# Optimization experiments

Hardware: AMD Instinct MI355X
Metric: run time of the kernel (lower is better)

## Reference

```python
import jax, jax.numpy as jnp
import numpy as np

N_NODES = 20000
N_EDGES = 160000
N_GRAPHS = 64
X_DIM = 9
E_DIM = 1
U_RAW = 4096
U_DIM = 256
E_HID = 1024
E_OUT = 512
N_HID = 512
N_OUT = 1


def _lin_params(k, fan_in, fan_out):
    kw, kb = jax.random.split(k)
    bound = 1.0 / np.sqrt(fan_in)
    W = jax.random.uniform(kw, (fan_in, fan_out), jnp.float32, -bound, bound)
    b = jax.random.uniform(kb, (fan_out,), jnp.float32, -bound, bound)
    return W, b


def setup_inputs() -> dict:
    key = jax.random.key(0)
    ks = jax.random.split(key, 16)
    x = jax.random.normal(ks[0], (N_NODES, X_DIM), jnp.float32)
    edge_attr = jax.random.normal(ks[1], (N_EDGES, E_DIM), jnp.float32)
    u = jax.random.normal(ks[2], (N_GRAPHS, U_RAW), jnp.float32)
    edge_index = jax.random.randint(ks[3], (2, N_EDGES), 0, N_NODES, jnp.int64)
    batch = jax.random.randint(ks[4], (N_NODES,), 0, N_GRAPHS, jnp.int64)

    Wsel, bsel = _lin_params(ks[5], U_RAW, U_DIM)
    e_in = E_DIM + 2 * X_DIM + U_DIM  # 275
    eW1, eb1 = _lin_params(ks[6], e_in, E_HID)
    eW2, eb2 = _lin_params(ks[7], E_HID, E_HID)
    eW3, eb3 = _lin_params(ks[8], E_HID, E_HID)
    eW4, eb4 = _lin_params(ks[9], E_HID, E_HID)
    eW5, eb5 = _lin_params(ks[10], E_HID, E_OUT)
    n1W1, n1b1 = _lin_params(ks[11], E_OUT + X_DIM, N_HID)  # 521
    n1W2, n1b2 = _lin_params(ks[12], N_HID, N_HID)
    n2W1, n2b1 = _lin_params(ks[13], X_DIM + N_HID + U_DIM, N_HID)  # 777
    n2W2, n2b2 = _lin_params(ks[14], N_HID, N_OUT)

    return dict(x=x, edge_attr=edge_attr, u=u, edge_index=edge_index, batch=batch,
                Wsel=Wsel, bsel=bsel,
                eW1=eW1, eb1=eb1, eW2=eW2, eb2=eb2, eW3=eW3, eb3=eb3,
                eW4=eW4, eb4=eb4, eW5=eW5, eb5=eb5,
                n1W1=n1W1, n1b1=n1b1, n1W2=n1W2, n1b2=n1b2,
                n2W1=n2W1, n2b1=n2b1, n2W2=n2W2, n2b2=n2b2)


def _forward(x, edge_attr, u, edge_index, batch,
             Wsel, bsel, eW1, eb1, eW2, eb2, eW3, eb3, eW4, eb4, eW5, eb5,
             n1W1, n1b1, n1W2, n1b2, n2W1, n2b1, n2W2, n2b2):
    relu = jax.nn.relu
    u2 = u @ Wsel + bsel  # [B, 256]
    row, col = edge_index[0], edge_index[1]

    # EdgeModel: cat([src, dest, edge_attr, u[batch[row]]]) -> 5-layer MLP
    e = jnp.concatenate([x[row], x[col], edge_attr, u2[batch[row]]], axis=1)
    e = relu(e @ eW1 + eb1)
    e = relu(e @ eW2 + eb2)
    e = relu(e @ eW3 + eb3)
    e = relu(e @ eW4 + eb4)
    e = e @ eW5 + eb5  # [E, 512]

    # NodeModel: gather x[col], MLP1, scatter_mean over row, MLP2
    h = jnp.concatenate([x[col], e], axis=1)
    h = relu(h @ n1W1 + n1b1)
    h = relu(h @ n1W2 + n1b2)  # [E, 512]
    ssum = jax.ops.segment_sum(h, row, num_segments=x.shape[0])
    cnt = jax.ops.segment_sum(jnp.ones((h.shape[0],), h.dtype), row, num_segments=x.shape[0])
    agg = ssum / jnp.maximum(cnt, 1.0)[:, None]  # scatter_mean

    z = jnp.concatenate([x, agg, u2[batch]], axis=1)
    z = relu(z @ n2W1 + n2b1)
    z = z @ n2W2 + n2b2  # [N, 1]
    return jnp.squeeze(z)


def reference(x, edge_attr, u, edge_index, batch,
              Wsel, bsel, eW1, eb1, eW2, eb2, eW3, eb3, eW4, eb4, eW5, eb5,
              n1W1, n1b1, n1W2, n1b2, n2W1, n2b1, n2W2, n2b2):
    return _forward(x, edge_attr, u, edge_index, batch,
                    Wsel, bsel, eW1, eb1, eW2, eb2, eW3, eb3, eW4, eb4, eW5, eb5,
                    n1W1, n1b1, n1W2, n1b2, n2W1, n2b1, n2W2, n2b2)
```

## Files before the change

kernel.cpp:

```cpp
#include <hip/hip_runtime.h>

typedef _Float16 f16;
typedef __attribute__((ext_vector_type(8))) _Float16 f16x8;
typedef __attribute__((ext_vector_type(4))) float f32x4;

#define E_TOTAL 160000
#define NN 20000
#define NGRAPH 64

__device__ __forceinline__ void gl_lds16(const void* g, void* l) {
    __builtin_amdgcn_global_load_lds((const __attribute__((address_space(1))) void*)g,
                                     (__attribute__((address_space(3))) void*)l, 16, 0, 0);
}

template <int RELU, int AUXU, int AUXX>
__global__ __launch_bounds__(256, 2) void hgemm(
    int M, int N, int K,
    const f16* __restrict__ A, int lda,
    const f16* __restrict__ Bt,
    f16* __restrict__ C, int ldc,
    const float* __restrict__ bias,
    const f16* __restrict__ utab, const int* __restrict__ uidx,
    const float* __restrict__ x9, const int* __restrict__ xidx, const float* __restrict__ W9)
{
    __shared__ __align__(16) char Ash[16384];
    __shared__ __align__(16) char Bsh[16384];
    __shared__ float Ws9[AUXX ? 1152 : 1];
    const int tid  = threadIdx.x;
    const int lane = tid & 63;
    const int w    = tid >> 6;
    const int bm = blockIdx.y * 128;
    const int bn = blockIdx.x * 128;
    const int wm = (w >> 1) * 64;
    const int wn = (w & 1) * 64;
    const int fr = lane & 15;
    const int kq = lane >> 4;

    const char* Ab = (const char*)A;
    const char* Bb = (const char*)Bt;
    const size_t lda2 = (size_t)lda * 2;
    const size_t ldb2 = (size_t)K * 2;

    f32x4 acc[4][4] = {};

    int srow[4], scb[4];
#pragma unroll
    for (int h = 0; h < 4; ++h) {
        int cch = w * 4 + h;
        int L = cch * 1024 + lane * 16;
        int row = L >> 7;
        srow[h] = row;
        scb[h] = (L & 127) ^ ((row & 7) << 4);
    }

    for (int k0 = 0; k0 < K; k0 += 64) {
        __syncthreads();
#pragma unroll
        for (int h = 0; h < 4; ++h) {
            int cch = w * 4 + h;
            gl_lds16(Ab + (size_t)(bm + srow[h]) * lda2 + (size_t)k0 * 2 + scb[h], Ash + cch * 1024);
            gl_lds16(Bb + (size_t)(bn + srow[h]) * ldb2 + (size_t)k0 * 2 + scb[h], Bsh + cch * 1024);
        }
        __syncthreads();
#pragma unroll
        for (int kk = 0; kk < 2; ++kk) {
            const int cb = (kk * 32 + kq * 8) * 2;
            f16x8 av[4], bv[4];
#pragma unroll
            for (int m = 0; m < 4; ++m) {
                int r = wm + m * 16 + fr;
                av[m] = *(const f16x8*)(Ash + r * 128 + (cb ^ ((r & 7) << 4)));
            }
#pragma unroll
            for (int n = 0; n < 4; ++n) {
                int r = wn + n * 16 + fr;
                bv[n] = *(const f16x8*)(Bsh + r * 128 + (cb ^ ((r & 7) << 4)));
            }
#pragma unroll
            for (int m = 0; m < 4; ++m)
#pragma unroll
                for (int n = 0; n < 4; ++n)
                    acc[m][n] = __builtin_amdgcn_mfma_f32_16x16x32_f16(av[m], bv[n], acc[m][n], 0, 0, 0);
        }
    }

    if (AUXX) {
        for (int t = tid; t < 9 * 128; t += 256)
            Ws9[t] = W9[(size_t)(t >> 7) * N + bn + (t & 127)];
        __syncthreads();
    }

#pragma unroll
    for (int m = 0; m < 4; ++m) {
        int r0 = bm + wm + m * 16 + kq * 4;
#pragma unroll
        for (int r = 0; r < 4; ++r) {
            int grow = r0 + r;
            if (grow >= M) continue;
            int ub = 0;
            if (AUXU) ub = uidx[grow];
            float xv[9];
            if (AUXX) {
                int xi = xidx ? xidx[grow] : grow;
#pragma unroll
                for (int q = 0; q < 9; ++q) xv[q] = x9[(size_t)xi * 9 + q];
            }
#pragma unroll
            for (int n = 0; n < 4; ++n) {
                int lcol = wn + n * 16 + fr;
                int col = bn + lcol;
                float v = acc[m][n][r] + bias[col];
                if (AUXU) v += (float)utab[(size_t)ub * N + col];
                if (AUXX) {
                    float s = 0.f;
#pragma unroll
                    for (int q = 0; q < 9; ++q) s = fmaf(xv[q], Ws9[q * 128 + lcol], s);
                    v += s;
                }
                if (RELU) v = fmaxf(v, 0.f);
                C[(size_t)grow * ldc + col] = (f16)v;
            }
        }
    }
}

__global__ void k_wt(const float* __restrict__ W, f16* __restrict__ Wt,
                     int r0, int Ksub, int N, int Kp)
{
    size_t t = (size_t)blockIdx.x * 256 + threadIdx.x;
    if (t >= (size_t)N * Kp) return;
    int n = (int)(t / Kp), k = (int)(t % Kp);
    Wt[t] = (k < Ksub) ? (f16)W[(size_t)(r0 + k) * N + n] : (f16)0.f;
}

__global__ __launch_bounds__(256) void k_u2(const float* __restrict__ u,
                                            const float* __restrict__ Wsel,
                                            const float* __restrict__ bsel,
                                            f16* __restrict__ u2h)
{
    __shared__ float us[4096];
    __shared__ float red[4][64];
    const int g = blockIdx.y;
    const int c0 = blockIdx.x * 64;
    const int col = threadIdx.x & 63;
    const int kp = threadIdx.x >> 6;
    for (int i = threadIdx.x; i < 4096; i += 256) us[i] = u[(size_t)g * 4096 + i];
    __syncthreads();
    float acc = 0.f;
    for (int k = kp * 1024; k < kp * 1024 + 1024; ++k)
        acc = fmaf(us[k], Wsel[(size_t)k * 256 + c0 + col], acc);
    red[kp][col] = acc;
    __syncthreads();
    if (kp == 0) {
        float v = red[0][col] + red[1][col] + red[2][col] + red[3][col] + bsel[c0 + col];
        u2h[(size_t)g * 256 + c0 + col] = (f16)v;
    }
}

__global__ void k_gather19(int e0, int Ce,
                           const float* __restrict__ x, const float* __restrict__ eattr,
                           const int* __restrict__ ei, const int* __restrict__ batch,
                           f16* __restrict__ feat, int* __restrict__ ebat)
{
    size_t t = (size_t)blockIdx.x * 256 + threadIdx.x;
    if (t >= (size_t)Ce * 64) return;
    int i = (int)(t >> 6), j = (int)(t & 63);
    int e = e0 + i;
    float v = 0.f;
    if (j < 9)        v = x[ei[e] * 9 + j];
    else if (j < 18)  v = x[ei[E_TOTAL + e] * 9 + (j - 9)];
    else if (j == 18) v = eattr[e];
    else if (j == 19) ebat[i] = batch[ei[e]];
    feat[t] = (f16)v;
}

__global__ void k_scatter(int e0, int Ce, const f16* __restrict__ h2,
                          const int* __restrict__ ei, float* __restrict__ ssum)
{
    size_t t = (size_t)blockIdx.x * 256 + threadIdx.x;
    if (t >= (size_t)Ce * 512) return;
    int i = (int)(t >> 9), j = (int)(t & 511);
    atomicAdd(ssum + (size_t)ei[e0 + i] * 512 + j, (float)h2[t]);
}

__global__ void k_cnt(const int* __restrict__ ei, float* __restrict__ cnt)
{
    int t = blockIdx.x * 256 + threadIdx.x;
    if (t < E_TOTAL) atomicAdd(cnt + ei[t], 1.0f);
}

__global__ void k_agg(const float* __restrict__ ssum, const float* __restrict__ cnt,
                      f16* __restrict__ agg)
{
    size_t t = (size_t)blockIdx.x * 256 + threadIdx.x;
    if (t >= (size_t)NN * 512) return;
    int n = (int)(t >> 9);
    agg[t] = (f16)(ssum[t] / fmaxf(cnt[n], 1.f));
}

__global__ void k_final(const f16* __restrict__ z1, const float* __restrict__ W,
                        const float* __restrict__ b, float* __restrict__ out)
{
    int gt = blockIdx.x * 256 + threadIdx.x;
    int row = gt >> 6;
    int lane = threadIdx.x & 63;
    if (row >= NN) return;
    float s = 0.f;
#pragma unroll
    for (int c = lane; c < 512; c += 64) s += (float)z1[(size_t)row * 512 + c] * W[c];
#pragma unroll
    for (int off = 32; off; off >>= 1) s += __shfl_down(s, off);
    if (lane == 0) out[row] = s + b[0];
}


extern "C" void kernel_launch(void* const* d_in, const int* in_sizes, int n_in,
                              void* d_out, int out_size, void* d_ws, size_t ws_size,
                              hipStream_t stream)
{
    const float* x     = (const float*)d_in[0];
    const float* eattr = (const float*)d_in[1];
    const float* u     = (const float*)d_in[2];
    const int*   ei    = (const int*)d_in[3];
    const int*   batch = (const int*)d_in[4];
    const float* Wsel  = (const float*)d_in[5];
    const float* bsel  = (const float*)d_in[6];
    const float* eW1 = (const float*)d_in[7],  * eb1 = (const float*)d_in[8];
    const float* eW2 = (const float*)d_in[9],  * eb2 = (const float*)d_in[10];
    const float* eW3 = (const float*)d_in[11], * eb3 = (const float*)d_in[12];
    const float* eW4 = (const float*)d_in[13], * eb4 = (const float*)d_in[14];
    const float* eW5 = (const float*)d_in[15], * eb5 = (const float*)d_in[16];
    const float* n1W1 = (const float*)d_in[17], * n1b1 = (const float*)d_in[18];
    const float* n1W2 = (const float*)d_in[19], * n1b2 = (const float*)d_in[20];
    const float* n2W1 = (const float*)d_in[21], * n2b1 = (const float*)d_in[22];
    const float* n2W2 = (const float*)d_in[23], * n2b2 = (const float*)d_in[24];
    float* out = (float*)d_out;

    char* ws = (char*)d_ws;
    size_t off = 0;
    auto alc = [&](size_t bytes) { char* p = ws + off; off += (bytes + 255) & ~(size_t)255; return p; };

    float* ssum  = (float*)alc((size_t)NN * 512 * 4);
    float* cnt   = (float*)alc((size_t)NN * 4);
    float* zbias = (float*)alc(1024 * 4);
    f16* u2h     = (f16*)alc((size_t)128 * 256 * 2);
    f16* ubias_e = (f16*)alc((size_t)64 * 1024 * 2);
    f16* ubias_n = (f16*)alc((size_t)64 * 512 * 2);
    f16* eW1t19  = (f16*)alc((size_t)1024 * 64 * 2);
    f16* eW1ut   = (f16*)alc((size_t)1024 * 256 * 2);
    f16* eW2t    = (f16*)alc((size_t)1024 * 1024 * 2);
    f16* eW3t    = (f16*)alc((size_t)1024 * 1024 * 2);
    f16* eW4t    = (f16*)alc((size_t)1024 * 1024 * 2);
    f16* eW5t    = (f16*)alc((size_t)512 * 1024 * 2);
    f16* n1W1et  = (f16*)alc((size_t)512 * 512 * 2);
    f16* n1W2t   = (f16*)alc((size_t)512 * 512 * 2);
    f16* n2W1et  = (f16*)alc((size_t)512 * 512 * 2);
    f16* n2W1ut  = (f16*)alc((size_t)512 * 256 * 2);
    f16* agg     = (f16*)alc((size_t)20096 * 512 * 2);
    f16* z1      = (f16*)alc((size_t)20096 * 512 * 2);
    size_t fixed = off;

    size_t per_edge = 64 * 2 + 1024 * 2 + 1024 * 2 + 4;
    size_t avail = ws_size > fixed ? ws_size - fixed : 0;
    long long Cll = (long long)(avail / per_edge);
    int C = (int)((Cll / 128) * 128);
    if (C > E_TOTAL) C = E_TOTAL;
    if (C < 128) C = 128;

    f16* featc = (f16*)(ws + fixed);
    f16* buf1  = featc + (size_t)C * 64;
    f16* buf2  = buf1 + (size_t)C * 1024;
    int* ebat  = (int*)(buf2 + (size_t)C * 1024);

    size_t zlen = (size_t)((char*)zbias - (char*)ssum) + 1024 * 4;
    hipMemsetAsync(ssum, 0, zlen, stream);

    auto wt = [&](const float* W, f16* Wt, int r0, int Ksub, int N, int Kp) {
        size_t tot = (size_t)N * Kp;
        k_wt<<<(unsigned)((tot + 255) / 256), 256, 0, stream>>>(W, Wt, r0, Ksub, N, Kp);
    };
    wt(eW1, eW1t19, 0, 19, 1024, 64);
    wt(eW1, eW1ut, 19, 256, 1024, 256);
    wt(eW2, eW2t, 0, 1024, 1024, 1024);
    wt(eW3, eW3t, 0, 1024, 1024, 1024);
    wt(eW4, eW4t, 0, 1024, 1024, 1024);
    wt(eW5, eW5t, 0, 1024, 512, 1024);
    wt(n1W1, n1W1et, 9, 512, 512, 512);
    wt(n1W2, n1W2t, 0, 512, 512, 512);
    wt(n2W1, n2W1et, 9, 512, 512, 512);
    wt(n2W1, n2W1ut, 521, 256, 512, 256);

    k_u2<<<dim3(4, NGRAPH), 256, 0, stream>>>(u, Wsel, bsel, u2h);
    k_cnt<<<(E_TOTAL + 255) / 256, 256, 0, stream>>>(ei, cnt);

    hgemm<0,0,0><<<dim3(8, 1), 256, 0, stream>>>(64, 1024, 256, u2h, 256, eW1ut,
        ubias_e, 1024, eb1, nullptr, nullptr, nullptr, nullptr, nullptr);
    hgemm<0,0,0><<<dim3(4, 1), 256, 0, stream>>>(64, 512, 256, u2h, 256, n2W1ut,
        ubias_n, 512, n2b1, nullptr, nullptr, nullptr, nullptr, nullptr);

    for (int e0 = 0; e0 < E_TOTAL; e0 += C) {
        int Ce = E_TOTAL - e0 < C ? E_TOTAL - e0 : C;
        int gy = (Ce + 127) / 128;

        k_gather19<<<(unsigned)(((size_t)Ce * 64 + 255) / 256), 256, 0, stream>>>(
            e0, Ce, x, eattr, ei, batch, featc, ebat);

        hgemm<1,1,0><<<dim3(8, gy), 256, 0, stream>>>(Ce, 1024, 64, featc, 64, eW1t19,
            buf1, 1024, zbias, ubias_e, ebat, nullptr, nullptr, nullptr);
        hgemm<1,0,0><<<dim3(8, gy), 256, 0, stream>>>(Ce, 1024, 1024, buf1, 1024, eW2t,
            buf2, 1024, eb2, nullptr, nullptr, nullptr, nullptr, nullptr);
        hgemm<1,0,0><<<dim3(8, gy), 256, 0, stream>>>(Ce, 1024, 1024, buf2, 1024, eW3t,
            buf1, 1024, eb3, nullptr, nullptr, nullptr, nullptr, nullptr);
        hgemm<1,0,0><<<dim3(8, gy), 256, 0, stream>>>(Ce, 1024, 1024, buf1, 1024, eW4t,
            buf2, 1024, eb4, nullptr, nullptr, nullptr, nullptr, nullptr);
        hgemm<0,0,0><<<dim3(4, gy), 256, 0, stream>>>(Ce, 512, 1024, buf2, 1024, eW5t,
            buf1, 512, eb5, nullptr, nullptr, nullptr, nullptr, nullptr);

        hgemm<1,0,1><<<dim3(4, gy), 256, 0, stream>>>(Ce, 512, 512, buf1, 512, n1W1et,
            buf2, 512, n1b1, nullptr, nullptr, x, ei + E_TOTAL + e0, n1W1);
        hgemm<1,0,0><<<dim3(4, gy), 256, 0, stream>>>(Ce, 512, 512, buf2, 512, n1W2t,
            buf1, 512, n1b2, nullptr, nullptr, nullptr, nullptr, nullptr);

        k_scatter<<<(unsigned)(((size_t)Ce * 512 + 255) / 256), 256, 0, stream>>>(
            e0, Ce, buf1, ei, ssum);
    }

    k_agg<<<(unsigned)(((size_t)NN * 512 + 255) / 256), 256, 0, stream>>>(ssum, cnt, agg);
    hgemm<1,1,1><<<dim3(4, 157), 256, 0, stream>>>(NN, 512, 512, agg, 512, n2W1et,
        z1, 512, zbias, ubias_n, batch, x, nullptr, n2W1);
    k_final<<<(NN * 64 + 255) / 256, 256, 0, stream>>>(z1, n2W2, n2b2, out);
}
```

Baseline: 2.588 ms.

## Enlarge GEMM tiles to 256x256 with 512 threads and double-buffered LDS

Replaces the 128x128 / 256-thread hgemm with a 256x256 / 512-thread variant. Each wave now computes a 128x64 sub-tile. LDS is double-buffered: the next K-slice is prefetched with global_load_lds while the current one feeds the MFMAs. Only one barrier per iteration remains, and s_setprio is raised around the MFMA block. The goal is more data reuse per tile and overlap of global loads with compute. In exchange, each block uses about 128KB of LDS, which limits occupancy. With a single barrier, a fast wave may start filling a buffer that slower waves are still reading. Small launches get fewer blocks, and workspace padding is adjusted to 256-row multiples.

```diff
diff --git a/kernel.cpp b/kernel.cpp
--- a/kernel.cpp
+++ b/kernel.cpp
@@ -14,7 +14,7 @@
 }
 
 template <int RELU, int AUXU, int AUXX>
-__global__ __launch_bounds__(256, 2) void hgemm(
+__global__ __launch_bounds__(512, 2) void hgemm2(
     int M, int N, int K,
     const f16* __restrict__ A, int lda,
     const f16* __restrict__ Bt,
@@ -23,16 +23,17 @@
     const f16* __restrict__ utab, const int* __restrict__ uidx,
     const float* __restrict__ x9, const int* __restrict__ xidx, const float* __restrict__ W9)
 {
-    __shared__ __align__(16) char Ash[16384];
-    __shared__ __align__(16) char Bsh[16384];
-    __shared__ float Ws9[AUXX ? 1152 : 1];
+    __shared__ __align__(16) char Ash[2][32768];
+    __shared__ __align__(16) char Bsh[2][32768];
+    __shared__ float Ws9[AUXX ? 2304 : 1];
+
     const int tid  = threadIdx.x;
     const int lane = tid & 63;
     const int w    = tid >> 6;
-    const int bm = blockIdx.y * 128;
-    const int bn = blockIdx.x * 128;
-    const int wm = (w >> 1) * 64;
-    const int wn = (w & 1) * 64;
+    const int bm = blockIdx.y * 256;
+    const int bn = blockIdx.x * 256;
+    const int wm = (w >> 2) * 128;
+    const int wn = (w & 3) * 64;
     const int fr = lane & 15;
     const int kq = lane >> 4;
 
@@ -41,58 +42,83 @@
     const size_t lda2 = (size_t)lda * 2;
     const size_t ldb2 = (size_t)K * 2;
 
-    f32x4 acc[4][4] = {};
-
-    int srow[4], scb[4];
-#pragma unroll
-    for (int h = 0; h < 4; ++h) {
-        int cch = w * 4 + h;
+    f32x4 acc[8][4] = {};
+
+    size_t offA[4], offB[4];
+    int ldsoff[4];
+#pragma unroll
+    for (int i = 0; i < 4; ++i) {
+        int cch = w * 4 + i;
         int L = cch * 1024 + lane * 16;
         int row = L >> 7;
-        srow[h] = row;
-        scb[h] = (L & 127) ^ ((row & 7) << 4);
-    }
-
-    for (int k0 = 0; k0 < K; k0 += 64) {
+        int scb = (L & 127) ^ ((row & 7) << 4);
+        offA[i] = (size_t)(bm + row) * lda2 + scb;
+        offB[i] = (size_t)(bn + row) * ldb2 + scb;
+        ldsoff[i] = cch * 1024;
+    }
+
+    const int NT = K >> 6;
+
+#pragma unroll
+    for (int i = 0; i < 4; ++i) gl_lds16(Ab + offA[i], Ash[0] + ldsoff[i]);
+#pragma unroll
+    for (int i = 0; i < 4; ++i) gl_lds16(Bb + offB[i], Bsh[0] + ldsoff[i]);
+
+    int cur = 0;
+    for (int t = 0; t < NT; ++t) {
+        if (t + 1 < NT) {
+            size_t kb = (size_t)(t + 1) << 7;
+#pragma unroll
+            for (int i = 0; i < 4; ++i) gl_lds16(Ab + offA[i] + kb, Ash[cur ^ 1] + ldsoff[i]);
+#pragma unroll
+            for (int i = 0; i < 4; ++i) gl_lds16(Bb + offB[i] + kb, Bsh[cur ^ 1] + ldsoff[i]);
+            asm volatile("s_waitcnt vmcnt(8)" ::: "memory");
+        } else {
+            asm volatile("s_waitcnt vmcnt(0)" ::: "memory");
+        }
+        __builtin_amdgcn_s_barrier();
+        __builtin_amdgcn_sched_barrier(0);
+
+        const char* As = Ash[cur];
+        const char* Bs = Bsh[cur];
+
+        f16x8 bv[2][4];
+#pragma unroll
+        for (int ks = 0; ks < 2; ++ks) {
+            const int cb = (ks * 32 + kq * 8) * 2;
+#pragma unroll
+            for (int ni = 0; ni < 4; ++ni) {
+                int r = wn + ni * 16 + fr;
+                bv[ks][ni] = *(const f16x8*)(Bs + r * 128 + (cb ^ ((r & 7) << 4)));
+            }
+        }
+        __builtin_amdgcn_s_setprio(1);
+#pragma unroll
+        for (int mi = 0; mi < 8; ++mi) {
+            int r = wm + mi * 16 + fr;
+            int sw = (r & 7) << 4;
+            f16x8 a0 = *(const f16x8*)(As + r * 128 + ((kq * 16) ^ sw));
+            f16x8 a1 = *(const f16x8*)(As + r * 128 + ((64 + kq * 16) ^ sw));
+#pragma unroll
+            for (int ni = 0; ni < 4; ++ni)
+                acc[mi][ni] = __builtin_amdgcn_mfma_f32_16x16x32_f16(a0, bv[0][ni], acc[mi][ni], 0, 0, 0);
+#pragma unroll
+            for (int ni = 0; ni < 4; ++ni)
+                acc[mi][ni] = __builtin_amdgcn_mfma_f32_16x16x32_f16(a1, bv[1][ni], acc[mi][ni], 0, 0, 0);
+        }
+        __builtin_amdgcn_s_setprio(0);
+        cur ^= 1;
+    }
+
+    if (AUXX) {
+        for (int t = tid; t < 9 * 256; t += 512)
+            Ws9[t] = W9[(size_t)(t >> 8) * N + bn + (t & 255)];
         __syncthreads();
-#pragma unroll
-        for (int h = 0; h < 4; ++h) {
-            int cch = w * 4 + h;
-            gl_lds16(Ab + (size_t)(bm + srow[h]) * lda2 + (size_t)k0 * 2 + scb[h], Ash + cch * 1024);
-            gl_lds16(Bb + (size_t)(bn + srow[h]) * ldb2 + (size_t)k0 * 2 + scb[h], Bsh + cch * 1024);
-        }
-        __syncthreads();
-#pragma unroll
-        for (int kk = 0; kk < 2; ++kk) {
-            const int cb = (kk * 32 + kq * 8) * 2;
-            f16x8 av[4], bv[4];
-#pragma unroll
-            for (int m = 0; m < 4; ++m) {
-                int r = wm + m * 16 + fr;
-                av[m] = *(const f16x8*)(Ash + r * 128 + (cb ^ ((r & 7) << 4)));
-            }
-#pragma unroll
-            for (int n = 0; n < 4; ++n) {
-                int r = wn + n * 16 + fr;
-                bv[n] = *(const f16x8*)(Bsh + r * 128 + (cb ^ ((r & 7) << 4)));
-            }
-#pragma unroll
-            for (int m = 0; m < 4; ++m)
-#pragma unroll
-                for (int n = 0; n < 4; ++n)
-                    acc[m][n] = __builtin_amdgcn_mfma_f32_16x16x32_f16(av[m], bv[n], acc[m][n], 0, 0, 0);
-        }
-    }
-
-    if (AUXX) {
-        for (int t = tid; t < 9 * 128; t += 256)
-            Ws9[t] = W9[(size_t)(t >> 7) * N + bn + (t & 127)];
-        __syncthreads();
-    }
-
-#pragma unroll
-    for (int m = 0; m < 4; ++m) {
-        int r0 = bm + wm + m * 16 + kq * 4;
+    }
+
+#pragma unroll
+    for (int mi = 0; mi < 8; ++mi) {
+        int r0 = bm + wm + mi * 16 + kq * 4;
 #pragma unroll
         for (int r = 0; r < 4; ++r) {
             int grow = r0 + r;
@@ -106,15 +132,15 @@
                 for (int q = 0; q < 9; ++q) xv[q] = x9[(size_t)xi * 9 + q];
             }
 #pragma unroll
-            for (int n = 0; n < 4; ++n) {
-                int lcol = wn + n * 16 + fr;
+            for (int ni = 0; ni < 4; ++ni) {
+                int lcol = wn + ni * 16 + fr;
                 int col = bn + lcol;
-                float v = acc[m][n][r] + bias[col];
+                float v = acc[mi][ni][r] + bias[col];
                 if (AUXU) v += (float)utab[(size_t)ub * N + col];
                 if (AUXX) {
                     float s = 0.f;
 #pragma unroll
-                    for (int q = 0; q < 9; ++q) s = fmaf(xv[q], Ws9[q * 128 + lcol], s);
+                    for (int q = 0; q < 9; ++q) s = fmaf(xv[q], Ws9[q * 256 + lcol], s);
                     v += s;
                 }
                 if (RELU) v = fmaxf(v, 0.f);
@@ -243,7 +269,7 @@
     float* ssum  = (float*)alc((size_t)NN * 512 * 4);
     float* cnt   = (float*)alc((size_t)NN * 4);
     float* zbias = (float*)alc(1024 * 4);
-    f16* u2h     = (f16*)alc((size_t)128 * 256 * 2);
+    f16* u2h     = (f16*)alc((size_t)256 * 256 * 2);
     f16* ubias_e = (f16*)alc((size_t)64 * 1024 * 2);
     f16* ubias_n = (f16*)alc((size_t)64 * 512 * 2);
     f16* eW1t19  = (f16*)alc((size_t)1024 * 64 * 2);
@@ -256,16 +282,16 @@
     f16* n1W2t   = (f16*)alc((size_t)512 * 512 * 2);
     f16* n2W1et  = (f16*)alc((size_t)512 * 512 * 2);
     f16* n2W1ut  = (f16*)alc((size_t)512 * 256 * 2);
-    f16* agg     = (f16*)alc((size_t)20096 * 512 * 2);
-    f16* z1      = (f16*)alc((size_t)20096 * 512 * 2);
+    f16* agg     = (f16*)alc((size_t)20224 * 512 * 2);
+    f16* z1      = (f16*)alc((size_t)20224 * 512 * 2);
     size_t fixed = off;
 
     size_t per_edge = 64 * 2 + 1024 * 2 + 1024 * 2 + 4;
     size_t avail = ws_size > fixed ? ws_size - fixed : 0;
     long long Cll = (long long)(avail / per_edge);
-    int C = (int)((Cll / 128) * 128);
+    int C = (int)((Cll / 256) * 256);
     if (C > E_TOTAL) C = E_TOTAL;
-    if (C < 128) C = 128;
+    if (C < 256) C = 256;
 
     f16* featc = (f16*)(ws + fixed);
     f16* buf1  = featc + (size_t)C * 64;
@@ -293,32 +319,32 @@
     k_u2<<<dim3(4, NGRAPH), 256, 0, stream>>>(u, Wsel, bsel, u2h);
     k_cnt<<<(E_TOTAL + 255) / 256, 256, 0, stream>>>(ei, cnt);
 
-    hgemm<0,0,0><<<dim3(8, 1), 256, 0, stream>>>(64, 1024, 256, u2h, 256, eW1ut,
+    hgemm2<0,0,0><<<dim3(4, 1), 512, 0, stream>>>(64, 1024, 256, u2h, 256, eW1ut,
         ubias_e, 1024, eb1, nullptr, nullptr, nullptr, nullptr, nullptr);
-    hgemm<0,0,0><<<dim3(4, 1), 256, 0, stream>>>(64, 512, 256, u2h, 256, n2W1ut,
+    hgemm2<0,0,0><<<dim3(2, 1), 512, 0, stream>>>(64, 512, 256, u2h, 256, n2W1ut,
         ubias_n, 512, n2b1, nullptr, nullptr, nullptr, nullptr, nullptr);
 
     for (int e0 = 0; e0 < E_TOTAL; e0 += C) {
         int Ce = E_TOTAL - e0 < C ? E_TOTAL - e0 : C;
-        int gy = (Ce + 127) / 128;
+        int gy = (Ce + 255) / 256;
 
         k_gather19<<<(unsigned)(((size_t)Ce * 64 + 255) / 256), 256, 0, stream>>>(
             e0, Ce, x, eattr, ei, batch, featc, ebat);
 
-        hgemm<1,1,0><<<dim3(8, gy), 256, 0, stream>>>(Ce, 1024, 64, featc, 64, eW1t19,
+        hgemm2<1,1,0><<<dim3(4, gy), 512, 0, stream>>>(Ce, 1024, 64, featc, 64, eW1t19,
             buf1, 1024, zbias, ubias_e, ebat, nullptr, nullptr, nullptr);
-        hgemm<1,0,0><<<dim3(8, gy), 256, 0, stream>>>(Ce, 1024, 1024, buf1, 1024, eW2t,
+        hgemm2<1,0,0><<<dim3(4, gy), 512, 0, stream>>>(Ce, 1024, 1024, buf1, 1024, eW2t,
             buf2, 1024, eb2, nullptr, nullptr, nullptr, nullptr, nullptr);
-        hgemm<1,0,0><<<dim3(8, gy), 256, 0, stream>>>(Ce, 1024, 1024, buf2, 1024, eW3t,
+        hgemm2<1,0,0><<<dim3(4, gy), 512, 0, stream>>>(Ce, 1024, 1024, buf2, 1024, eW3t,
             buf1, 1024, eb3, nullptr, nullptr, nullptr, nullptr, nullptr);
-        hgemm<1,0,0><<<dim3(8, gy), 256, 0, stream>>>(Ce, 1024, 1024, buf1, 1024, eW4t,
+        hgemm2<1,0,0><<<dim3(4, gy), 512, 0, stream>>>(Ce, 1024, 1024, buf1, 1024, eW4t,
             buf2, 1024, eb4, nullptr, nullptr, nullptr, nullptr, nullptr);
-        hgemm<0,0,0><<<dim3(4, gy), 256, 0, stream>>>(Ce, 512, 1024, buf2, 1024, eW5t,
+        hgemm2<0,0,0><<<dim3(2, gy), 512, 0, stream>>>(Ce, 512, 1024, buf2, 1024, eW5t,
             buf1, 512, eb5, nullptr, nullptr, nullptr, nullptr, nullptr);
 
-        hgemm<1,0,1><<<dim3(4, gy), 256, 0, stream>>>(Ce, 512, 512, buf1, 512, n1W1et,
+        hgemm2<1,0,1><<<dim3(2, gy), 512, 0, stream>>>(Ce, 512, 512, buf1, 512, n1W1et,
             buf2, 512, n1b1, nullptr, nullptr, x, ei + E_TOTAL + e0, n1W1);
-        hgemm<1,0,0><<<dim3(4, gy), 256, 0, stream>>>(Ce, 512, 512, buf2, 512, n1W2t,
+        hgemm2<1,0,0><<<dim3(2, gy), 512, 0, stream>>>(Ce, 512, 512, buf2, 512, n1W2t,
             buf1, 512, n1b2, nullptr, nullptr, nullptr, nullptr, nullptr);
 
         k_scatter<<<(unsigned)(((size_t)Ce * 512 + 255) / 256), 256, 0, stream>>>(
@@ -326,7 +352,7 @@
     }
 
     k_agg<<<(unsigned)(((size_t)NN * 512 + 255) / 256), 256, 0, stream>>>(ssum, cnt, agg);
-    hgemm<1,1,1><<<dim3(4, 157), 256, 0, stream>>>(NN, 512, 512, agg, 512, n2W1et,
+    hgemm2<1,1,1><<<dim3(2, 79), 512, 0, stream>>>(NN, 512, 512, agg, 512, n2W1et,
         z1, 512, zbias, ubias_n, batch, x, nullptr, n2W1);
     k_final<<<(NN * 64 + 255) / 256, 256, 0, stream>>>(z1, n2W2, n2b2, out);
 }
```

After: 2.697 ms. 1.04x slower.
